# Kernel optimization log

Measured on AMD Instinct MI355X. Metric: run time of the kernel, lower is better.

Reference implementation:

```python
import jax, jax.numpy as jnp
import numpy as np

B, N, C = 8, 1024, 768
H = 12
HD = C // H  # 64
SCALE = C ** (-0.5)  # NOTE: source scales by n_emb^-0.5, not head_dim^-0.5


def setup_inputs() -> dict:
    key = jax.random.key(0)
    k1, k2, k3 = jax.random.split(key, 3)
    x = jax.random.normal(k1, (B, N, C), dtype=jnp.float32)
    W_qkv = jax.random.normal(k2, (C, 3 * C), dtype=jnp.float32) * (C ** -0.5)
    b_qkv = jnp.zeros((3 * C,), dtype=jnp.float32)
    W_proj = jax.random.normal(k3, (C, C), dtype=jnp.float32) * (C ** -0.5)
    b_proj = jnp.zeros((C,), dtype=jnp.float32)
    return {"x": x, "W_qkv": W_qkv, "b_qkv": b_qkv, "W_proj": W_proj, "b_proj": b_proj}


def reference(x, W_qkv, b_qkv, W_proj, b_proj):
    # qkv projection: (B,N,3C) -> (3,B,H,N,HD)
    qkv = x @ W_qkv + b_qkv
    qkv = qkv.reshape(B, N, 3, H, HD).transpose(2, 0, 3, 1, 4)
    q, k, v = qkv[0], qkv[1], qkv[2]
    # scaled dot-product attention (full N x N, as in source)
    attn = jnp.einsum("bhnd,bhmd->bhnm", q, k) * SCALE
    attn = jax.nn.softmax(attn, axis=-1)
    out = jnp.einsum("bhnm,bhmd->bhnd", attn, v)
    out = out.transpose(0, 2, 1, 3).reshape(B, N, C)
    return out @ W_proj + b_proj
```

## Files before the change

kernel.cpp:

```cpp
#include <hip/hip_runtime.h>
#include <hip/hip_bf16.h>
#include <stdint.h>

#define Bb 8
#define Nn_ 1024
#define Cc_ 768
#define Hh 12
#define HDd 64
#define BHh 96
#define SCALE_F 0.03608439182435161f
#define CL2F (0.03608439182435161f * 1.4426950408889634f)

typedef __attribute__((ext_vector_type(4))) float f32x4;
typedef __attribute__((ext_vector_type(8))) __bf16 bf16x8;

__device__ __forceinline__ unsigned short f2bf(float f) {
  uint32_t u = __builtin_bit_cast(uint32_t, f);
  uint32_t r = (u + 0x7fffu + ((u >> 16) & 1u)) >> 16;
  return (unsigned short)r;
}

__device__ __forceinline__ uint32_t cvtpk(float a, float b) {
  uint32_t r;
  asm("v_cvt_pk_bf16_f32 %0, %1, %2" : "=v"(r) : "v"(a), "v"(b));
  return r;
}

__device__ __forceinline__ f32x4 mfma16(bf16x8 a, bf16x8 b, f32x4 c) {
  return __builtin_amdgcn_mfma_f32_16x16x32_bf16(a, b, c, 0, 0, 0);
}

typedef const __attribute__((address_space(1))) uint32_t* gas1_t;
typedef __attribute__((address_space(3))) uint32_t* las3_t;
__device__ __forceinline__ void gl_lds16(const void* g, void* l) {
  __builtin_amdgcn_global_load_lds((gas1_t)g, (las3_t)l, 16, 0, 0);
}

#define VMCNT(n) asm volatile("s_waitcnt vmcnt(" #n ")" ::: "memory")
#define SBAR() __builtin_amdgcn_s_barrier()
#define SCHED_FENCE() __builtin_amdgcn_sched_barrier(0)

__global__ __launch_bounds__(256) void k_pre(
    const float* __restrict__ x, unsigned short* __restrict__ xb,
    const float* __restrict__ Wqkv, unsigned short* __restrict__ wqt,
    const float* __restrict__ Wproj, unsigned short* __restrict__ wpt) {
  __shared__ unsigned short tile[64][65];
  int b = blockIdx.x, t = threadIdx.x;
  if (b < 6144) {
    int i = b * 256 + t;
    float4 v = ((const float4*)x)[i];
    ushort4 o;
    o.x = f2bf(v.x); o.y = f2bf(v.y); o.z = f2bf(v.z); o.w = f2bf(v.w);
    ((ushort4*)xb)[i] = o;
    return;
  }
  const float* src;
  unsigned short* dst;
  int CC, bx, by;
  if (b < 6576) {
    int bb = b - 6144;
    bx = bb % 36; by = bb / 36; src = Wqkv; dst = wqt; CC = 2304;
  } else {
    int bb = b - 6576;
    bx = bb % 12; by = bb / 12; src = Wproj; dst = wpt; CC = 768;
  }
  int c0 = bx * 64, r0 = by * 64;
#pragma unroll
  for (int i = 0; i < 16; ++i) {
    int idx = t + 256 * i;
    int r = idx >> 6, c = idx & 63;
    tile[r][c] = f2bf(src[(size_t)(r0 + r) * CC + c0 + c]);
  }
  __syncthreads();
#pragma unroll
  for (int i = 0; i < 16; ++i) {
    int idx = t + 256 * i;
    int a = idx >> 6, bq = idx & 63;
    dst[(size_t)(c0 + a) * 768 + r0 + bq] = tile[bq][a];
  }
}

template <int EPI, int BMt, int BNt, int MINB>
__global__ __launch_bounds__(256, MINB) void k_gemm(
    const unsigned short* __restrict__ A, const unsigned short* __restrict__ Bt,
    const float* __restrict__ bias, float* __restrict__ out,
    unsigned short* __restrict__ Qb, unsigned short* __restrict__ Kb,
    unsigned short* __restrict__ Vtb, int Nw) {
  constexpr int WGM = (BNt == 128) ? 2 : 4;
  constexpr int WM = BMt / WGM;
  constexpr int MR = WM / 16;
  constexpr int AL = BMt / 32;
  constexpr int BL = BNt / 32;
  constexpr int ASZ = BMt * 128;
  constexpr int BUFSZ = ASZ + BNt * 128;
  __shared__ char smem[2 * BUFSZ];
  int t = threadIdx.x;
  int w = t >> 6, lane = t & 63;
  int g = lane >> 4, l15 = lane & 15;
  int bid = blockIdx.x;
  int m0 = ((bid & 7) * 8 + ((bid >> 3) & 7)) * BMt;
  int n0 = (bid >> 6) * BNt;
  int wr = (BNt == 128) ? (w >> 1) : w;
  int wc = (BNt == 128) ? (w & 1) : 0;

  f32x4 acc[MR][4] = {};

  const char* gA[AL];
  const char* gB[BL];
  int sA[AL], sB[BL];
#pragma unroll
  for (int it = 0; it < AL; ++it) {
    int off = it * 4096 + t * 16;
    int row = off >> 7;
    int sb = (off & 127) ^ ((row & 7) << 4);
    gA[it] = (const char*)A + (size_t)(m0 + row) * 1536 + sb;
    sA[it] = it * 4096 + w * 1024;
  }
#pragma unroll
  for (int it = 0; it < BL; ++it) {
    int off = it * 4096 + t * 16;
    int row = off >> 7;
    int sb = (off & 127) ^ ((row & 7) << 4);
    gB[it] = (const char*)Bt + (size_t)(n0 + row) * 1536 + sb;
    sB[it] = ASZ + it * 4096 + w * 1024;
  }

  auto STG = [&](int buf, int kt) {
    char* base = smem + buf * BUFSZ;
#pragma unroll
    for (int it = 0; it < AL; ++it) gl_lds16(gA[it] + kt * 128, base + sA[it]);
#pragma unroll
    for (int it = 0; it < BL; ++it) gl_lds16(gB[it] + kt * 128, base + sB[it]);
  };

  const char *pa[2][MR], *pb[2][4];
#pragma unroll
  for (int ks = 0; ks < 2; ++ks) {
    int kb = ks * 64 + g * 16;
#pragma unroll
    for (int mi = 0; mi < MR; ++mi) {
      int rowA = wr * WM + mi * 16 + l15;
      pa[ks][mi] = smem + rowA * 128 + (kb ^ ((rowA & 7) << 4));
    }
#pragma unroll
    for (int ni = 0; ni < 4; ++ni) {
      int rowB = wc * 64 + ni * 16 + l15;
      pb[ks][ni] = smem + ASZ + rowB * 128 + (kb ^ ((rowB & 7) << 4));
    }
  }

  STG(0, 0);
#pragma unroll
  for (int kt = 0; kt < 12; ++kt) {
    int off = (kt & 1) * BUFSZ;
    if (kt < 11) {
      STG((kt & 1) ^ 1, kt + 1);
      if constexpr (BL == 4) { VMCNT(8); } else { VMCNT(6); }
    } else {
      VMCNT(0);
    }
    SBAR();
    SCHED_FENCE();
    bf16x8 av[2][MR], bv[2][4];
#pragma unroll
    for (int ks = 0; ks < 2; ++ks) {
#pragma unroll
      for (int mi = 0; mi < MR; ++mi) av[ks][mi] = *(const bf16x8*)(pa[ks][mi] + off);
#pragma unroll
      for (int ni = 0; ni < 4; ++ni) bv[ks][ni] = *(const bf16x8*)(pb[ks][ni] + off);
    }
#pragma unroll
    for (int ks = 0; ks < 2; ++ks)
#pragma unroll
      for (int mi = 0; mi < MR; ++mi)
#pragma unroll
        for (int ni = 0; ni < 4; ++ni)
          acc[mi][ni] = mfma16(av[ks][mi], bv[ks][ni], acc[mi][ni]);
    SCHED_FENCE();
    if (kt < 11) SBAR();
  }

  if constexpr (EPI == 0) {
#pragma unroll
    for (int mi = 0; mi < MR; ++mi) {
#pragma unroll
      for (int ni = 0; ni < 4; ++ni) {
        int col = n0 + wc * 64 + ni * 16 + l15;
        float bvs = bias[col];
#pragma unroll
        for (int j = 0; j < 4; ++j) {
          int row = m0 + wr * WM + mi * 16 + g * 4 + j;
          out[(size_t)row * Nw + col] = acc[mi][ni][j] + bvs;
        }
      }
    }
  } else {
    int typ = n0 / 768;
    int hh = (n0 % 768) >> 6;
    int bI = m0 >> 10;
    int bh = bI * 12 + hh;
    int nbase = m0 & 1023;
    if (typ < 2) {
      unsigned short* dst = (typ == 0) ? Qb : Kb;
#pragma unroll
      for (int mi = 0; mi < MR; ++mi) {
#pragma unroll
        for (int ni = 0; ni < 4; ++ni) {
          int d = ni * 16 + l15;
          float bvs = bias[n0 + d];
#pragma unroll
          for (int j = 0; j < 4; ++j) {
            int n = nbase + wr * WM + mi * 16 + g * 4 + j;
            dst[((size_t)bh * 1024 + n) * 64 + d] = f2bf(acc[mi][ni][j] + bvs);
          }
        }
      }
    } else {
      __syncthreads();
      unsigned short(*tile)[136] = reinterpret_cast<unsigned short(*)[136]>(smem);
#pragma unroll
      for (int mi = 0; mi < MR; ++mi) {
#pragma unroll
        for (int ni = 0; ni < 4; ++ni) {
          int d = ni * 16 + l15;
          float bvs = bias[n0 + d];
#pragma unroll
          for (int j = 0; j < 4; ++j) {
            int nloc = wr * WM + mi * 16 + g * 4 + j;
            tile[d][nloc] = f2bf(acc[mi][ni][j] + bvs);
          }
        }
      }
      __syncthreads();
#pragma unroll
      for (int i = 0; i < 4; ++i) {
        int c = t + i * 256;
        int d = c >> 4, off = (c & 15) * 8;
        uint4 vdat = *(const uint4*)&tile[d][off];
        *(uint4*)(Vtb + ((size_t)bh * 64 + d) * 1024 + nbase + off) = vdat;
      }
    }
  }
}

__global__ __launch_bounds__(256, 3) void k_attn(
    const unsigned short* __restrict__ Q, const unsigned short* __restrict__ K,
    const unsigned short* __restrict__ Vt, unsigned short* __restrict__ Oa) {
  __shared__ char smem[49152];
  char* Ks = smem;
  char* Ps = smem + 32768;
  int t = threadIdx.x, w = t >> 6, lane = t & 63;
  int g = lane >> 4, l15 = lane & 15;

  int fb = blockIdx.x;
  int bh = (fb & 7) * 12 + ((fb >> 3) % 12);
  int n0 = (fb / 96) * 128;
  int bI = bh / 12, h = bh % 12;
  char* Pw = Ps + w * 4096;

  bf16x8 qf[2][2];
  {
    const char* qbase = (const char*)Q + ((size_t)bh * 1024 + n0 + w * 32 + l15) * 128 + g * 16;
    qf[0][0] = *(const bf16x8*)(qbase);
    qf[0][1] = *(const bf16x8*)(qbase + 64);
    qf[1][0] = *(const bf16x8*)(qbase + 16 * 128);
    qf[1][1] = *(const bf16x8*)(qbase + 16 * 128 + 64);
  }

  f32x4 acc[2][4] = {};
  float lrun[2] = {0.f, 0.f};

  const char* pK[2][4];
#pragma unroll
  for (int ks = 0; ks < 2; ++ks)
#pragma unroll
    for (int ff = 0; ff < 4; ++ff) {
      int row = ff * 16 + l15;
      pK[ks][ff] = Ks + row * 128 + ((ks * 64 + g * 16) ^ ((row & 7) << 4));
    }
  char* pPw[2][4];
  const char* pPr[2][2];
#pragma unroll
  for (int q = 0; q < 2; ++q) {
    int prow = q * 16 + l15, swz = (l15 & 7) << 4;
#pragma unroll
    for (int ff = 0; ff < 4; ++ff) pPw[q][ff] = Pw + prow * 128 + ((ff * 32 + g * 8) ^ swz);
#pragma unroll
    for (int ks = 0; ks < 2; ++ks) pPr[q][ks] = Pw + prow * 128 + ((ks * 64 + g * 16) ^ swz);
  }

  int o0 = t * 16, o1 = t * 16 + 4096;
  int r0 = o0 >> 7, r1 = o1 >> 7;
  int sb0 = (o0 & 127) ^ ((r0 & 7) << 4);
  int sb1 = (o1 & 127) ^ ((r1 & 7) << 4);
  const char* KgA = (const char*)K + (size_t)bh * 131072 + (size_t)r0 * 128 + sb0;
  const char* KgB = (const char*)K + (size_t)bh * 131072 + (size_t)r1 * 128 + sb1;
  const char* VgA = (const char*)Vt + (size_t)bh * 131072 + (size_t)r0 * 2048 + sb0;
  const char* VgB = (const char*)Vt + (size_t)bh * 131072 + (size_t)r1 * 2048 + sb1;

  auto STG = [&](int buf, int mt) {
    char* Kd = Ks + buf * 8192;
    char* Vd = Ks + 16384 + buf * 8192;
    gl_lds16(KgA + (size_t)mt * 8192, Kd + w * 1024);
    gl_lds16(KgB + (size_t)mt * 8192, Kd + 4096 + w * 1024);
    gl_lds16(VgA + (size_t)mt * 128, Vd + w * 1024);
    gl_lds16(VgB + (size_t)mt * 128, Vd + 4096 + w * 1024);
  };

  auto TILE = [&](int off) {
    f32x4 s[4][2] = {};
#pragma unroll
    for (int ks = 0; ks < 2; ++ks)
#pragma unroll
      for (int ff = 0; ff < 4; ++ff) {
        bf16x8 kv = *(const bf16x8*)(pK[ks][ff] + off);
        s[ff][0] = mfma16(kv, qf[0][ks], s[ff][0]);
        s[ff][1] = mfma16(kv, qf[1][ks], s[ff][1]);
      }

#pragma unroll
    for (int q = 0; q < 2; ++q) {
      float rs = 0.f;
#pragma unroll
      for (int ff = 0; ff < 4; ++ff) {
        float p0 = __builtin_amdgcn_exp2f(s[ff][q][0] * CL2F);
        float p1 = __builtin_amdgcn_exp2f(s[ff][q][1] * CL2F);
        float p2 = __builtin_amdgcn_exp2f(s[ff][q][2] * CL2F);
        float p3 = __builtin_amdgcn_exp2f(s[ff][q][3] * CL2F);
        rs += (p0 + p1) + (p2 + p3);
        uint2 pk;
        pk.x = cvtpk(p0, p1);
        pk.y = cvtpk(p2, p3);
        *(uint2*)(pPw[q][ff]) = pk;
      }
      lrun[q] += rs;
    }

#pragma unroll
    for (int ks = 0; ks < 2; ++ks) {
      bf16x8 pa0 = *(const bf16x8*)(pPr[0][ks]);
      bf16x8 pa1 = *(const bf16x8*)(pPr[1][ks]);
#pragma unroll
      for (int fd = 0; fd < 4; ++fd) {
        bf16x8 vv = *(const bf16x8*)(pK[ks][fd] + 16384 + off);
        acc[0][fd] = mfma16(pa0, vv, acc[0][fd]);
        acc[1][fd] = mfma16(pa1, vv, acc[1][fd]);
      }
    }
  };

  STG(0, 0);
  for (int mt2 = 0; mt2 < 8; ++mt2) {
    STG(1, 2 * mt2 + 1);
    VMCNT(4);
    SBAR();
    SCHED_FENCE();
    TILE(0);
    SCHED_FENCE();
    SBAR();
    if (mt2 < 7) {
      STG(0, 2 * mt2 + 2);
      VMCNT(4);
    } else {
      VMCNT(0);
    }
    SBAR();
    SCHED_FENCE();
    TILE(8192);
    SCHED_FENCE();
    if (mt2 < 7) SBAR();
  }

#pragma unroll
  for (int q = 0; q < 2; ++q) {
    float l = lrun[q];
    l += __shfl_xor(l, 16, 64);
    l += __shfl_xor(l, 32, 64);
    lrun[q] = l;
  }
#pragma unroll
  for (int q = 0; q < 2; ++q) {
#pragma unroll
    for (int j = 0; j < 4; ++j) {
      float lv = __shfl(lrun[q], g * 4 + j, 64);
      float inv = 1.0f / lv;
      int n = n0 + w * 32 + q * 16 + g * 4 + j;
      size_t rowb = ((size_t)bI * 1024 + n) * 768 + h * 64;
#pragma unroll
      for (int fd = 0; fd < 4; ++fd)
        Oa[rowb + fd * 16 + l15] = (unsigned short)(cvtpk(acc[q][fd][j] * inv, 0.f) & 0xffffu);
    }
  }
}

extern "C" void kernel_launch(void* const* d_in, const int* in_sizes, int n_in,
                              void* d_out, int out_size, void* d_ws, size_t ws_size,
                              hipStream_t stream) {
  const float* x = (const float*)d_in[0];
  const float* Wqkv = (const float*)d_in[1];
  const float* bqkv = (const float*)d_in[2];
  const float* Wproj = (const float*)d_in[3];
  const float* bproj = (const float*)d_in[4];
  float* out = (float*)d_out;

  char* ws = (char*)d_ws;
  unsigned short* xb  = (unsigned short*)(ws);
  unsigned short* wqt = (unsigned short*)(ws + 12582912);
  unsigned short* wpt = (unsigned short*)(ws + 16121856);
  unsigned short* Qb  = (unsigned short*)(ws + 17301504);
  unsigned short* Kb  = (unsigned short*)(ws + 29884416);
  unsigned short* Vtb = (unsigned short*)(ws + 42467328);
  unsigned short* Oa  = (unsigned short*)(ws + 55050240);

  k_pre<<<dim3(6720), dim3(256), 0, stream>>>(x, xb, Wqkv, wqt, Wproj, wpt);
  k_gemm<1, 128, 64, 3><<<dim3(2304), dim3(256), 0, stream>>>(xb, wqt, bqkv, nullptr,
                                                              Qb, Kb, Vtb, 2304);
  k_attn<<<dim3(768), dim3(256), 0, stream>>>(Qb, Kb, Vtb, Oa);
  k_gemm<0, 128, 64, 3><<<dim3(768), dim3(256), 0, stream>>>(Oa, wpt, bproj, out,
                                                             nullptr, nullptr, nullptr, 768);
}
```

Before: 98.41 us.

## Triple-buffer GEMM K-loop with one barrier per iteration

Moves the GEMM from double to triple buffering in LDS. Tiles kt and kt+1 are prefetched up front, the load for kt+2 is issued after the barrier, and the trailing barrier in each iteration is removed. This hides more global-load latency and halves barrier count. In exchange LDS use per block grows by half, and the launch bounds drop from 3 to 2 blocks per CU, which may reduce occupancy. Unused BNt==128 warp-layout code is also removed.

```diff
diff --git a/kernel.cpp b/kernel.cpp
--- a/kernel.cpp
+++ b/kernel.cpp
@@ -80,28 +80,25 @@
   }
 }
 
-template <int EPI, int BMt, int BNt, int MINB>
-__global__ __launch_bounds__(256, MINB) void k_gemm(
+template <int EPI, int BMt, int BNt>
+__global__ __launch_bounds__(256, 2) void k_gemm(
     const unsigned short* __restrict__ A, const unsigned short* __restrict__ Bt,
     const float* __restrict__ bias, float* __restrict__ out,
     unsigned short* __restrict__ Qb, unsigned short* __restrict__ Kb,
     unsigned short* __restrict__ Vtb, int Nw) {
-  constexpr int WGM = (BNt == 128) ? 2 : 4;
-  constexpr int WM = BMt / WGM;
+  constexpr int WM = BMt / 4;
   constexpr int MR = WM / 16;
   constexpr int AL = BMt / 32;
   constexpr int BL = BNt / 32;
   constexpr int ASZ = BMt * 128;
   constexpr int BUFSZ = ASZ + BNt * 128;
-  __shared__ char smem[2 * BUFSZ];
+  __shared__ char smem[3 * BUFSZ];
   int t = threadIdx.x;
   int w = t >> 6, lane = t & 63;
   int g = lane >> 4, l15 = lane & 15;
   int bid = blockIdx.x;
   int m0 = ((bid & 7) * 8 + ((bid >> 3) & 7)) * BMt;
   int n0 = (bid >> 6) * BNt;
-  int wr = (BNt == 128) ? (w >> 1) : w;
-  int wc = (BNt == 128) ? (w & 1) : 0;
 
   f32x4 acc[MR][4] = {};
 
@@ -139,28 +136,25 @@
     int kb = ks * 64 + g * 16;
 #pragma unroll
     for (int mi = 0; mi < MR; ++mi) {
-      int rowA = wr * WM + mi * 16 + l15;
+      int rowA = w * WM + mi * 16 + l15;
       pa[ks][mi] = smem + rowA * 128 + (kb ^ ((rowA & 7) << 4));
     }
 #pragma unroll
     for (int ni = 0; ni < 4; ++ni) {
-      int rowB = wc * 64 + ni * 16 + l15;
+      int rowB = ni * 16 + l15;
       pb[ks][ni] = smem + ASZ + rowB * 128 + (kb ^ ((rowB & 7) << 4));
     }
   }
 
   STG(0, 0);
+  STG(1, 1);
 #pragma unroll
   for (int kt = 0; kt < 12; ++kt) {
-    int off = (kt & 1) * BUFSZ;
-    if (kt < 11) {
-      STG((kt & 1) ^ 1, kt + 1);
-      if constexpr (BL == 4) { VMCNT(8); } else { VMCNT(6); }
-    } else {
-      VMCNT(0);
-    }
+    if (kt < 11) { VMCNT(6); } else { VMCNT(0); }
     SBAR();
     SCHED_FENCE();
+    if (kt + 2 < 12) STG((kt + 2) % 3, kt + 2);
+    int off = (kt % 3) * BUFSZ;
     bf16x8 av[2][MR], bv[2][4];
 #pragma unroll
     for (int ks = 0; ks < 2; ++ks) {
@@ -177,7 +171,6 @@
         for (int ni = 0; ni < 4; ++ni)
           acc[mi][ni] = mfma16(av[ks][mi], bv[ks][ni], acc[mi][ni]);
     SCHED_FENCE();
-    if (kt < 11) SBAR();
   }
 
   if constexpr (EPI == 0) {
@@ -185,11 +178,11 @@
     for (int mi = 0; mi < MR; ++mi) {
 #pragma unroll
       for (int ni = 0; ni < 4; ++ni) {
-        int col = n0 + wc * 64 + ni * 16 + l15;
+        int col = n0 + ni * 16 + l15;
         float bvs = bias[col];
 #pragma unroll
         for (int j = 0; j < 4; ++j) {
-          int row = m0 + wr * WM + mi * 16 + g * 4 + j;
+          int row = m0 + w * WM + mi * 16 + g * 4 + j;
           out[(size_t)row * Nw + col] = acc[mi][ni][j] + bvs;
         }
       }
@@ -210,7 +203,7 @@
           float bvs = bias[n0 + d];
 #pragma unroll
           for (int j = 0; j < 4; ++j) {
-            int n = nbase + wr * WM + mi * 16 + g * 4 + j;
+            int n = nbase + w * WM + mi * 16 + g * 4 + j;
             dst[((size_t)bh * 1024 + n) * 64 + d] = f2bf(acc[mi][ni][j] + bvs);
           }
         }
@@ -226,7 +219,7 @@
           float bvs = bias[n0 + d];
 #pragma unroll
           for (int j = 0; j < 4; ++j) {
-            int nloc = wr * WM + mi * 16 + g * 4 + j;
+            int nloc = w * WM + mi * 16 + g * 4 + j;
             tile[d][nloc] = f2bf(acc[mi][ni][j] + bvs);
           }
         }
@@ -413,9 +406,9 @@
   unsigned short* Oa  = (unsigned short*)(ws + 55050240);
 
   k_pre<<<dim3(6720), dim3(256), 0, stream>>>(x, xb, Wqkv, wqt, Wproj, wpt);
-  k_gemm<1, 128, 64, 3><<<dim3(2304), dim3(256), 0, stream>>>(xb, wqt, bqkv, nullptr,
-                                                              Qb, Kb, Vtb, 2304);
+  k_gemm<1, 128, 64><<<dim3(2304), dim3(256), 0, stream>>>(xb, wqt, bqkv, nullptr,
+                                                           Qb, Kb, Vtb, 2304);
   k_attn<<<dim3(768), dim3(256), 0, stream>>>(Qb, Kb, Vtb, Oa);
-  k_gemm<0, 128, 64, 3><<<dim3(768), dim3(256), 0, stream>>>(Oa, wpt, bproj, out,
-                                                             nullptr, nullptr, nullptr, 768);
-}
+  k_gemm<0, 128, 64><<<dim3(768), dim3(256), 0, stream>>>(Oa, wpt, bproj, out,
+                                                          nullptr, nullptr, nullptr, 768);
+}
```

Result: no change. 100.3 us (+2.0%).
